# Kernel tuning notes

Hardware: AMD Instinct MI355X
Metric: run time of the kernel (lower is better)

The kernel has to match this reference:

```python
import jax, jax.numpy as jnp
import numpy as np

N_NODES = 50000
NEG_SLOPE = 0.2


def gat_conv(x, src, dst, W, al, ar, b):
    """DGL-style GATConv. x:[N,Fin] W:[Fin,H*D] al,ar:[H,D] b:[H*D] -> [N,H,D]."""
    H, D = al.shape
    feat = (x @ W).reshape(-1, H, D)                      # [N,H,D]
    el = jnp.sum(feat * al, axis=-1)                      # [N,H]
    er = jnp.sum(feat * ar, axis=-1)                      # [N,H]
    e = jax.nn.leaky_relu(el[src] + er[dst], NEG_SLOPE)   # [E,H] per-edge scores
    # segment softmax over incoming edges of each dst node
    m = jax.ops.segment_max(e, dst, num_segments=N_NODES)  # [N,H] (-inf for empty)
    ex = jnp.exp(e - m[dst])                              # [E,H]
    s = jax.ops.segment_sum(ex, dst, num_segments=N_NODES)  # [N,H]
    alpha = ex / s[dst]                                   # [E,H]
    msg = alpha[:, :, None] * feat[src]                   # [E,H,D]
    out = jax.ops.segment_sum(msg, dst, num_segments=N_NODES)  # [N,H,D]
    return out + b.reshape(1, H, D)


def setup_inputs() -> dict:
    key = jax.random.key(0)
    ks = jax.random.split(key, 12)
    E = 800000
    inp = {
        "x": jax.random.normal(ks[0], (N_NODES, 128), jnp.float32),
        "W1": jax.random.normal(ks[1], (2, 128, 128), jnp.float32) * 0.1,
        "al1": jax.random.normal(ks[2], (2, 4, 32), jnp.float32) * 0.1,
        "ar1": jax.random.normal(ks[3], (2, 4, 32), jnp.float32) * 0.1,
        "b1": jnp.zeros((2, 128), jnp.float32),
        "W2": jax.random.normal(ks[4], (2, 128, 64), jnp.float32) * 0.1,
        "al2": jax.random.normal(ks[5], (2, 1, 64), jnp.float32) * 0.1,
        "ar2": jax.random.normal(ks[6], (2, 1, 64), jnp.float32) * 0.1,
        "b2": jnp.zeros((2, 64), jnp.float32),
        "src": jax.random.randint(ks[7], (2, E), 0, N_NODES, jnp.int32),
        "dst": jax.random.randint(ks[8], (2, E), 0, N_NODES, jnp.int32),
    }
    return inp


def reference(x, W1, al1, ar1, b1, W2, al2, ar2, b2, src, dst):
    R = src.shape[0]  # number of meta-path relations
    # layer 1: HeteroGraphConv(sum over relations) -> elu(flatten heads)
    h1 = sum(gat_conv(x, src[r], dst[r], W1[r], al1[r], ar1[r], b1[r])
             for r in range(R))                           # [N,4,32]
    h1 = jax.nn.elu(h1.reshape(N_NODES, -1))              # [N,128]
    # layer 2: single head, mean over head dim
    h2 = sum(gat_conv(h1, src[r], dst[r], W2[r], al2[r], ar2[r], b2[r])
             for r in range(R))                           # [N,1,64]
    return jnp.mean(h2, axis=1)                           # [N,64]
```

## Files before the change

### kernel.cpp

```cpp
#include <hip/hip_runtime.h>
#include <hip/hip_bf16.h>
#include <math.h>

using bf16x8 = __attribute__((ext_vector_type(8))) short;
using f32x4  = __attribute__((ext_vector_type(4))) float;
using v4i    = __attribute__((ext_vector_type(4))) int;

#define NCH 32
#define SCAN_B 1024

__device__ __forceinline__ float b2f(unsigned short u) {
    return __uint_as_float(((unsigned)u) << 16);
}
__device__ __forceinline__ unsigned short f2b(float f) {
    unsigned u = __float_as_uint(f);
    return (unsigned short)((u + 0x7fff + ((u >> 16) & 1)) >> 16);
}

__global__ void k_prep(const float* __restrict__ x, unsigned short* __restrict__ xb, int n8,
                       const float* __restrict__ W1, const float* __restrict__ W2,
                       unsigned short* __restrict__ wt1, unsigned short* __restrict__ wt2,
                       unsigned* __restrict__ cnt, int ncnt, int nbx, int nbw) {
    int bid = blockIdx.x;
    if (bid < nbx) {
        int i = bid * 256 + threadIdx.x;
        if (i >= n8) return;
        float4 a = ((const float4*)x)[i * 2], b = ((const float4*)x)[i * 2 + 1];
        uint4 o;
        o.x = f2b(a.x) | ((unsigned)f2b(a.y) << 16);
        o.y = f2b(a.z) | ((unsigned)f2b(a.w) << 16);
        o.z = f2b(b.x) | ((unsigned)f2b(b.y) << 16);
        o.w = f2b(b.z) | ((unsigned)f2b(b.w) << 16);
        ((uint4*)xb)[i] = o;
    } else if (bid < nbx + nbw) {
        int i = (bid - nbx) * 256 + threadIdx.x;
        if (i < 32768) {
            int r = i >> 14, c = (i >> 7) & 127, k = i & 127;
            wt1[i] = f2b(W1[(r << 14) + (k << 7) + c]);
        } else {
            int j = i - 32768;
            if (j >= 16384) return;
            int r = j >> 13, c = (j >> 7) & 63, k = j & 127;
            wt2[j] = f2b(W2[r * 8192 + k * 64 + c]);
        }
    } else {
        int i = (bid - nbx - nbw) * 256 + threadIdx.x;
        if (i < ncnt) cnt[i] = 0u;
    }
}

__global__ __launch_bounds__(256) void k_histp(const int* __restrict__ dst,
                                               unsigned* __restrict__ cnt, int E, int N) {
    __shared__ unsigned sm[6250];
    const int part = blockIdx.x & 7, chunk = blockIdx.x >> 3;
    const int r = blockIdx.y;
    const int P = N / 8;
    const int lo = part * P;
    for (int i = threadIdx.x; i < P; i += 256) sm[i] = 0u;
    __syncthreads();
    const int per = E / NCH;
    const int e0 = chunk * per, e1 = e0 + per;
    const int* dr = dst + (size_t)r * E;
    for (int e = e0 + (int)threadIdx.x * 4; e < e1; e += 1024) {
        v4i d4 = *(const v4i*)(dr + e);
        int a0 = d4.x - lo, a1 = d4.y - lo, a2 = d4.z - lo, a3 = d4.w - lo;
        if ((unsigned)a0 < (unsigned)P) atomicAdd(&sm[a0], 1u);
        if ((unsigned)a1 < (unsigned)P) atomicAdd(&sm[a1], 1u);
        if ((unsigned)a2 < (unsigned)P) atomicAdd(&sm[a2], 1u);
        if ((unsigned)a3 < (unsigned)P) atomicAdd(&sm[a3], 1u);
    }
    __syncthreads();
    unsigned* cr = cnt + (size_t)r * N + lo;
    for (int i = threadIdx.x; i < P; i += 256) {
        unsigned v = sm[i];
        if (v) atomicAdd(&cr[i], v);
    }
}

__global__ void k_scanA(const unsigned* __restrict__ cnt, unsigned* __restrict__ bsum,
                        int n, int nb) {
    int r = blockIdx.y, b = blockIdx.x;
    int i0 = b * SCAN_B;
    unsigned s = 0;
    for (int t = threadIdx.x; t < SCAN_B; t += 256) {
        int i = i0 + t;
        if (i < n) s += cnt[(size_t)r * n + i];
    }
    __shared__ unsigned red[256];
    red[threadIdx.x] = s; __syncthreads();
    for (int st = 128; st > 0; st >>= 1) {
        if ((int)threadIdx.x < st) red[threadIdx.x] += red[threadIdx.x + st];
        __syncthreads();
    }
    if (threadIdx.x == 0) bsum[r * nb + b] = red[0];
}

__global__ void k_scanC2(unsigned* __restrict__ cnt, const unsigned* __restrict__ bsum,
                         unsigned* __restrict__ off, int n, int nb) {
    int r = blockIdx.y, b = blockIdx.x;
    __shared__ unsigned sbase[65];
    if (threadIdx.x < 64) {
        int l = threadIdx.x;
        unsigned orig = (l < nb) ? bsum[r * nb + l] : 0u;
        unsigned v = orig;
        for (int st = 1; st < 64; st <<= 1) {
            unsigned t = __shfl_up(v, st);
            if (l >= st) v += t;
        }
        sbase[l] = v - orig;
        if (l == 63) sbase[64] = v;
    }
    __syncthreads();
    if (b == 0 && threadIdx.x == 0) off[(size_t)r * (n + 1) + n] = sbase[64];
    const unsigned base = sbase[b];
    int i0 = b * SCAN_B + (int)threadIdx.x * 4;
    unsigned v[4]; unsigned s = 0;
#pragma unroll
    for (int j = 0; j < 4; j++) {
        int i = i0 + j;
        v[j] = (i < n) ? cnt[(size_t)r * n + i] : 0u;
        s += v[j];
    }
    __shared__ unsigned red[256];
    red[threadIdx.x] = s; __syncthreads();
    for (int st = 1; st < 256; st <<= 1) {
        unsigned t = ((int)threadIdx.x >= st) ? red[threadIdx.x - st] : 0u;
        __syncthreads();
        red[threadIdx.x] += t;
        __syncthreads();
    }
    unsigned run = base + red[threadIdx.x] - s;
#pragma unroll
    for (int j = 0; j < 4; j++) {
        int i = i0 + j;
        if (i < n) {
            off[(size_t)r * (n + 1) + i] = run;
            cnt[(size_t)r * n + i] = run;
        }
        run += v[j];
    }
}

__device__ __forceinline__ void scat_body(int bid, const int* __restrict__ src,
                                          const int* __restrict__ dst, unsigned* __restrict__ cur,
                                          unsigned short* __restrict__ csr, int E, int N) {
    const int part = bid & 7;
    const int q = bid >> 3;
    const int r = q & 1, chunk = q >> 1;
    const int lo = part * (N / 8), hi = lo + N / 8;
    const int per = E / NCH;
    const int e0 = chunk * per, e1 = e0 + per;
    const int* dr = dst + (size_t)r * E;
    const int* sr = src + (size_t)r * E;
    unsigned* curr = cur + (size_t)r * N;
    unsigned short* csrr = csr + (size_t)r * E;
    for (int e = e0 + (int)threadIdx.x * 4; e < e1; e += 1024) {
        v4i d4 = *(const v4i*)(dr + e);
        bool m0 = (d4.x >= lo) & (d4.x < hi);
        bool m1 = (d4.y >= lo) & (d4.y < hi);
        bool m2 = (d4.z >= lo) & (d4.z < hi);
        bool m3 = (d4.w >= lo) & (d4.w < hi);
        if (m0 | m1 | m2 | m3) {
            v4i s4 = *(const v4i*)(sr + e);
            if (m0) { unsigned p = atomicAdd(&curr[d4.x], 1u);
                      __builtin_nontemporal_store((unsigned short)s4.x, &csrr[p]); }
            if (m1) { unsigned p = atomicAdd(&curr[d4.y], 1u);
                      __builtin_nontemporal_store((unsigned short)s4.y, &csrr[p]); }
            if (m2) { unsigned p = atomicAdd(&curr[d4.z], 1u);
                      __builtin_nontemporal_store((unsigned short)s4.z, &csrr[p]); }
            if (m3) { unsigned p = atomicAdd(&curr[d4.w], 1u);
                      __builtin_nontemporal_store((unsigned short)s4.w, &csrr[p]); }
        }
    }
}

template <int M, int H>
__device__ __forceinline__ void gemm_body(int xblk, int r,
        const unsigned short* __restrict__ Xb, const unsigned short* __restrict__ Wt0,
        const float* __restrict__ alv, const float* __restrict__ arv,
        unsigned short* __restrict__ feat0, float* __restrict__ el, float* __restrict__ er,
        int N, unsigned short* xs, unsigned short* ws) {
    constexpr int D = M / H;
    const unsigned short* Wt = Wt0 + (size_t)r * M * 128;
    unsigned short* outp = feat0 + (size_t)r * N * M;
    float* elr = el + (size_t)r * N * H;
    float* err = er + (size_t)r * N * H;
    const int tid = threadIdx.x;
    const int row0 = xblk * 64;
    for (int ch = tid; ch < 64 * 16; ch += 256) {
        int rr = ch >> 4, c16 = ch & 15;
        int gr = row0 + rr;
        uint4 v = make_uint4(0, 0, 0, 0);
        if (gr < N) v = ((const uint4*)(Xb + (size_t)gr * 128))[c16];
        int byte = rr * 256 + ((c16 * 16) ^ ((rr & 7) << 4));
        *(uint4*)((char*)xs + byte) = v;
    }
    for (int ch = tid; ch < M * 16; ch += 256) {
        int rr = ch >> 4, c16 = ch & 15;
        uint4 v = ((const uint4*)(Wt + (size_t)rr * 128))[c16];
        int byte = rr * 256 + ((c16 * 16) ^ ((rr & 7) << 4));
        *(uint4*)((char*)ws + byte) = v;
    }
    __syncthreads();
    const int w = tid >> 6, l = tid & 63;
    const int sub = l & 15;
    const int ar_ = w * 16 + sub;
    const int kg = l >> 4;
    bf16x8 a[4];
#pragma unroll
    for (int k4 = 0; k4 < 4; k4++) {
        int byte = ar_ * 256 + (((kg * 16) + k4 * 64) ^ ((ar_ & 7) << 4));
        a[k4] = *(const bf16x8*)((const char*)xs + byte);
    }
    float alr[M / 16], arr[M / 16];
#pragma unroll
    for (int ct = 0; ct < M / 16; ct++) {
        alr[ct] = alv[(size_t)r * M + ct * 16 + sub];
        arr[ct] = arv[(size_t)r * M + ct * 16 + sub];
    }
    float pel[H][4], per[H][4];
#pragma unroll
    for (int h = 0; h < H; h++)
#pragma unroll
        for (int q = 0; q < 4; q++) { pel[h][q] = 0.f; per[h][q] = 0.f; }

#pragma unroll
    for (int ct = 0; ct < M / 16; ct++) {
        f32x4 acc = {0.f, 0.f, 0.f, 0.f};
        const int bc = ct * 16 + sub;
#pragma unroll
        for (int k4 = 0; k4 < 4; k4++) {
            int byte = bc * 256 + (((kg * 16) + k4 * 64) ^ ((bc & 7) << 4));
            bf16x8 bfr = *(const bf16x8*)((const char*)ws + byte);
            acc = __builtin_amdgcn_mfma_f32_16x16x32_bf16(a[k4], bfr, acc, 0, 0, 0);
        }
        const int hct = (ct * 16) / D;
#pragma unroll
        for (int q = 0; q < 4; q++) {
            pel[hct][q] += acc[q] * alr[ct];
            per[hct][q] += acc[q] * arr[ct];
        }
#pragma unroll
        for (int q = 0; q < 4; q++) {
            int gr = row0 + w * 16 + kg * 4 + q;
            if (gr < N) outp[(size_t)gr * M + ct * 16 + sub] = f2b(acc[q]);
        }
    }
#pragma unroll
    for (int h = 0; h < H; h++)
#pragma unroll
        for (int q = 0; q < 4; q++) {
            float v = pel[h][q], u = per[h][q];
#pragma unroll
            for (int o = 8; o > 0; o >>= 1) { v += __shfl_xor(v, o); u += __shfl_xor(u, o); }
            pel[h][q] = v; per[h][q] = u;
        }
#pragma unroll
    for (int h = 0; h < H; h++) {
        if (sub == h) {
#pragma unroll
            for (int q = 0; q < 4; q++) {
                int gr = row0 + w * 16 + kg * 4 + q;
                if (gr < N) { elr[(size_t)gr * H + h] = pel[h][q]; err[(size_t)gr * H + h] = per[h][q]; }
            }
        }
    }
}

__global__ __launch_bounds__(256) void k_scatgemm(
    const int* __restrict__ src, const int* __restrict__ dst,
    unsigned* __restrict__ cur, unsigned short* __restrict__ csr, int E, int N, int scatBlocks,
    const unsigned short* __restrict__ Xb, const unsigned short* __restrict__ Wt0,
    const float* __restrict__ alv, const float* __restrict__ arv,
    unsigned short* __restrict__ feat0, float* __restrict__ el, float* __restrict__ er) {
    __shared__ __align__(16) unsigned short xs[64 * 128];
    __shared__ __align__(16) unsigned short ws[128 * 128];
    int bid = blockIdx.x;
    if (bid < scatBlocks) {
        scat_body(bid, src, dst, cur, csr, E, N);
    } else {
        int g = bid - scatBlocks;
        gemm_body<128, 4>(g >> 1, g & 1, Xb, Wt0, alv, arv, feat0, el, er, N, xs, ws);
    }
}

__global__ __launch_bounds__(256) void k_gemm2(
    const unsigned short* __restrict__ Xb, const unsigned short* __restrict__ Wt0,
    const float* __restrict__ alv, const float* __restrict__ arv,
    unsigned short* __restrict__ feat0, float* __restrict__ el, float* __restrict__ er, int N) {
    __shared__ __align__(16) unsigned short xs[64 * 128];
    __shared__ __align__(16) unsigned short ws[64 * 128];
    gemm_body<64, 1>(blockIdx.x, blockIdx.y, Xb, Wt0, alv, arv, feat0, el, er, N, xs, ws);
}

template <int ELUF>
__global__ __launch_bounds__(256) void k_node_gat1(
    const unsigned* __restrict__ off, const unsigned short* __restrict__ csr_src,
    const float* __restrict__ el, const float* __restrict__ er,
    const unsigned short* __restrict__ feat0, const unsigned short* __restrict__ feat1,
    const float* __restrict__ bias, unsigned* __restrict__ outp, int N, int E) {
    constexpr int H = 4, HD = 128;
    __shared__ float s_w[4][4 * 64];
    __shared__ int s_sid[4][64];
    const int wslot = threadIdx.x >> 6;
    const int lane = threadIdx.x & 63;
    const int n = (blockIdx.x * 256 + threadIdx.x) >> 6;
    if (n >= N) return;
    const int c0 = lane * 2;
    const int h = c0 / 32;
    const unsigned laneoff = (unsigned)lane << 2;

    float res[2] = {0.f, 0.f};

    for (int r = 0; r < 2; r++) {
        const char* __restrict__ featc = (const char*)(r ? feat1 : feat0);
        const float* elr = el + (size_t)r * N * H;
        const float* ernp = er + (size_t)r * N * H + (size_t)n * H;
        float ern[H];
#pragma unroll
        for (int hh = 0; hh < H; hh++) ern[hh] = ernp[hh];
        const unsigned* offr = off + (size_t)r * (N + 1);
        const unsigned short* srcs = csr_src + (size_t)r * E;
        const unsigned o0 = offr[n], o1 = offr[n + 1];

        float den = 0.f;
        float acc[2] = {0.f, 0.f};

        for (unsigned base = o0; base < o1; base += 64) {
            const int cnt = (int)min(64u, o1 - base);
            if (lane < cnt) {
                unsigned sv = srcs[base + lane];
                s_sid[wslot][lane] = (int)sv;
                float4 e4 = *(const float4*)(elr + (size_t)sv * 4);
                float v0 = e4.x + ern[0]; v0 = v0 > 0.f ? v0 : 0.2f * v0;
                float v1 = e4.y + ern[1]; v1 = v1 > 0.f ? v1 : 0.2f * v1;
                float v2 = e4.z + ern[2]; v2 = v2 > 0.f ? v2 : 0.2f * v2;
                float v3 = e4.w + ern[3]; v3 = v3 > 0.f ? v3 : 0.2f * v3;
                float4 wv = make_float4(__expf(v0), __expf(v1), __expf(v2), __expf(v3));
                *(float4*)&s_w[wslot][lane * 4] = wv;
            }
            asm volatile("s_waitcnt lgkmcnt(0)" ::: "memory");
#pragma unroll 8
            for (int j = 0; j < cnt; j++) {
                unsigned sv = (unsigned)s_sid[wslot][j];
                float wv = s_w[wslot][j * 4 + h];
                den += wv;
                unsigned u = *(const unsigned*)(featc + ((sv << 8) + laneoff));
                acc[0] += wv * __uint_as_float(u << 16);
                acc[1] += wv * __uint_as_float(u & 0xffff0000u);
            }
        }
        if (den > 0.f) {
            float inv = 1.f / den;
            res[0] += acc[0] * inv;
            res[1] += acc[1] * inv;
        }
    }
    float v0 = res[0] + bias[c0] + bias[HD + c0];
    float v1 = res[1] + bias[c0 + 1] + bias[HD + c0 + 1];
    if (ELUF) { v0 = v0 > 0.f ? v0 : expm1f(v0); v1 = v1 > 0.f ? v1 : expm1f(v1); }
    outp[((size_t)n * HD + c0) / 2] = f2b(v0) | ((unsigned)f2b(v1) << 16);
}

__global__ __launch_bounds__(256) void k_node_gat2(
    const unsigned* __restrict__ off, const unsigned short* __restrict__ csr_src,
    const float* __restrict__ el, const float* __restrict__ er,
    const unsigned short* __restrict__ feat0, const unsigned short* __restrict__ feat1,
    const float* __restrict__ bias, float* __restrict__ outp, int N, int E) {
    __shared__ uint2 s_ws[4][64];
    const int wslot = threadIdx.x >> 6;
    const int lane = threadIdx.x & 63;
    const int n = (blockIdx.x * 256 + threadIdx.x) >> 6;
    if (n >= N) return;
    const int sub = lane & 31, half = lane >> 5;
    const unsigned laneoff = (unsigned)sub << 2;

    float res[2] = {0.f, 0.f};

    for (int r = 0; r < 2; r++) {
        const char* __restrict__ featc = (const char*)(r ? feat1 : feat0);
        const float* elr = el + (size_t)r * N;
        const float ern = er[(size_t)r * N + n];
        const unsigned* offr = off + (size_t)r * (N + 1);
        const unsigned short* srcs = csr_src + (size_t)r * E;
        const unsigned o0 = offr[n], o1 = offr[n + 1];

        float den = 0.f;
        float acc[2] = {0.f, 0.f};

        for (unsigned base = o0; base < o1; base += 64) {
            const int cnt = (int)min(64u, o1 - base);
            if (lane < cnt) {
                unsigned sv = srcs[base + lane];
                float v = elr[sv] + ern; v = v > 0.f ? v : 0.2f * v;
                s_ws[wslot][lane] = make_uint2(sv, __float_as_uint(__expf(v)));
            }
            asm volatile("s_waitcnt lgkmcnt(0)" ::: "memory");
#pragma unroll 4
            for (int j2 = 0; j2 < cnt; j2 += 2) {
                int jj = j2 + half;
                int jjc = jj < cnt ? jj : 0;
                uint2 sw = s_ws[wslot][jjc];
                float wv = (jj < cnt) ? __uint_as_float(sw.y) : 0.f;
                den += wv;
                unsigned u = *(const unsigned*)(featc + (((size_t)sw.x << 7) + laneoff));
                acc[0] += wv * __uint_as_float(u << 16);
                acc[1] += wv * __uint_as_float(u & 0xffff0000u);
            }
        }
        acc[0] += __shfl_xor(acc[0], 32);
        acc[1] += __shfl_xor(acc[1], 32);
        den += __shfl_xor(den, 32);
        if (den > 0.f) {
            float inv = 1.f / den;
            res[0] += acc[0] * inv;
            res[1] += acc[1] * inv;
        }
    }
    if (half == 0) {
        int c = sub * 2;
        float v0 = res[0] + bias[c] + bias[64 + c];
        float v1 = res[1] + bias[c + 1] + bias[64 + c + 1];
        *(float2*)(outp + (size_t)n * 64 + c) = make_float2(v0, v1);
    }
}

extern "C" void kernel_launch(void* const* d_in, const int* in_sizes, int n_in,
                              void* d_out, int out_size, void* d_ws, size_t ws_size,
                              hipStream_t stream) {
    const float* x   = (const float*)d_in[0];
    const float* W1  = (const float*)d_in[1];
    const float* al1 = (const float*)d_in[2];
    const float* ar1 = (const float*)d_in[3];
    const float* b1  = (const float*)d_in[4];
    const float* W2  = (const float*)d_in[5];
    const float* al2 = (const float*)d_in[6];
    const float* ar2 = (const float*)d_in[7];
    const float* b2  = (const float*)d_in[8];
    const int* src   = (const int*)d_in[9];
    const int* dst   = (const int*)d_in[10];

    const int N = in_sizes[0] / 128;
    const int E = in_sizes[9] / 2;
    float* out = (float*)d_out;

    char* w = (char*)d_ws;
    unsigned short* xb   = (unsigned short*)w; w += (size_t)N * 128 * 2;
    unsigned short* feat = (unsigned short*)w; w += (size_t)2 * N * 128 * 2;
    unsigned short* h1b  = (unsigned short*)w; w += (size_t)N * 128 * 2;
    unsigned short* wt1  = (unsigned short*)w; w += (size_t)2 * 128 * 128 * 2;
    unsigned short* wt2  = (unsigned short*)w; w += (size_t)2 * 64 * 128 * 2;
    float* el      = (float*)w; w += (size_t)2 * N * 4 * 4;
    float* er      = (float*)w; w += (size_t)2 * N * 4 * 4;
    unsigned* cnt  = (unsigned*)w; w += (size_t)2 * N * 4;
    unsigned* off  = (unsigned*)w; w += (size_t)2 * (N + 1) * 4;
    unsigned* bsum = (unsigned*)w; w += 2 * 64 * 4;
    unsigned short* csr_src = (unsigned short*)w; w += (size_t)2 * E * 2;

    auto cdiv = [](long long a, long long b) { return (int)((a + b - 1) / b); };
    const int NB = cdiv(N, SCAN_B);

    const int nbx = cdiv((long long)N * 16, 256);
    const int nbw = cdiv(49152, 256);
    const int nbz = cdiv(2LL * N, 256);
    k_prep<<<nbx + nbw + nbz, 256, 0, stream>>>(x, xb, N * 16, W1, W2, wt1, wt2, cnt, 2 * N, nbx, nbw);

    { dim3 g(NCH * 8, 2); k_histp<<<g, 256, 0, stream>>>(dst, cnt, E, N); }
    { dim3 g(NB, 2); k_scanA<<<g, 256, 0, stream>>>(cnt, bsum, N, NB); }
    { dim3 g(NB, 2); k_scanC2<<<g, 256, 0, stream>>>(cnt, bsum, off, N, NB); }

    const int scatBlocks = NCH * 8 * 2;
    const int gemmBlocks = cdiv(N, 64) * 2;
    k_scatgemm<<<scatBlocks + gemmBlocks, 256, 0, stream>>>(
        src, dst, cnt, csr_src, E, N, scatBlocks, xb, wt1, al1, ar1, feat, el, er);

    k_node_gat1<1><<<cdiv(N, 4), 256, 0, stream>>>(off, csr_src, el, er,
        feat, feat + (size_t)N * 128, b1, (unsigned*)h1b, N, E);

    { dim3 g(cdiv(N, 64), 2);
      k_gemm2<<<g, 256, 0, stream>>>(h1b, wt2, al2, ar2, feat, el, er, N); }
    k_node_gat2<<<cdiv(N, 4), 256, 0, stream>>>(off, csr_src, el, er,
        feat, feat + (size_t)N * 64, b2, out, N, E);
}
```

Measured before the change: 244.7 us.

## Process four edges per wave in layer-2 aggregation and raise scatter chunk count

The layer-2 node aggregation kernel now splits each 64-lane wave into four 16-lane groups. Each lane loads 8 bytes (four bf16 features) per edge, so four edges are handled per iteration instead of two. The partial sums are then reduced with two cross-lane shuffles and written back as float4. Separately, NCH is doubled to 64, which changes the scatter/GEMM block count and chunking in the hidden kernel, while the histogram kernel is pinned to the old 32 chunks. This raises the number of edge loads in flight per wave but adds a shuffle step and may change scatter behaviour.

After: 255.6 us. 1.04x slower.

```diff
diff --git a/kernel.cpp b/kernel.cpp
--- a/kernel.cpp
+++ b/kernel.cpp
@@ -6,7 +6,7 @@
 using f32x4  = __attribute__((ext_vector_type(4))) float;
 using v4i    = __attribute__((ext_vector_type(4))) int;
 
-#define NCH 32
+#define NCH 64
 #define SCAN_B 1024
 
 __device__ __forceinline__ float b2f(unsigned short u) {
@@ -58,7 +58,7 @@
     const int lo = part * P;
     for (int i = threadIdx.x; i < P; i += 256) sm[i] = 0u;
     __syncthreads();
-    const int per = E / NCH;
+    const int per = E / 32;
     const int e0 = chunk * per, e1 = e0 + per;
     const int* dr = dst + (size_t)r * E;
     for (int e = e0 + (int)threadIdx.x * 4; e < e1; e += 1024) {
@@ -372,10 +372,10 @@
     const int lane = threadIdx.x & 63;
     const int n = (blockIdx.x * 256 + threadIdx.x) >> 6;
     if (n >= N) return;
-    const int sub = lane & 31, half = lane >> 5;
-    const unsigned laneoff = (unsigned)sub << 2;
-
-    float res[2] = {0.f, 0.f};
+    const int sub = lane & 15, quarter = lane >> 4;
+    const unsigned laneoff = (unsigned)sub << 3;
+
+    float res[4] = {0.f, 0.f, 0.f, 0.f};
 
     for (int r = 0; r < 2; r++) {
         const char* __restrict__ featc = (const char*)(r ? feat1 : feat0);
@@ -386,7 +386,7 @@
         const unsigned o0 = offr[n], o1 = offr[n + 1];
 
         float den = 0.f;
-        float acc[2] = {0.f, 0.f};
+        float acc[4] = {0.f, 0.f, 0.f, 0.f};
 
         for (unsigned base = o0; base < o1; base += 64) {
             const int cnt = (int)min(64u, o1 - base);
@@ -397,31 +397,40 @@
             }
             asm volatile("s_waitcnt lgkmcnt(0)" ::: "memory");
 #pragma unroll 4
-            for (int j2 = 0; j2 < cnt; j2 += 2) {
-                int jj = j2 + half;
+            for (int j4 = 0; j4 < cnt; j4 += 4) {
+                int jj = j4 + quarter;
                 int jjc = jj < cnt ? jj : 0;
                 uint2 sw = s_ws[wslot][jjc];
                 float wv = (jj < cnt) ? __uint_as_float(sw.y) : 0.f;
                 den += wv;
-                unsigned u = *(const unsigned*)(featc + (((size_t)sw.x << 7) + laneoff));
-                acc[0] += wv * __uint_as_float(u << 16);
-                acc[1] += wv * __uint_as_float(u & 0xffff0000u);
+                uint2 u = *(const uint2*)(featc + (((size_t)sw.x << 7) + laneoff));
+                acc[0] += wv * __uint_as_float(u.x << 16);
+                acc[1] += wv * __uint_as_float(u.x & 0xffff0000u);
+                acc[2] += wv * __uint_as_float(u.y << 16);
+                acc[3] += wv * __uint_as_float(u.y & 0xffff0000u);
             }
         }
-        acc[0] += __shfl_xor(acc[0], 32);
-        acc[1] += __shfl_xor(acc[1], 32);
+#pragma unroll
+        for (int f = 0; f < 4; f++) {
+            acc[f] += __shfl_xor(acc[f], 16);
+            acc[f] += __shfl_xor(acc[f], 32);
+        }
+        den += __shfl_xor(den, 16);
         den += __shfl_xor(den, 32);
         if (den > 0.f) {
             float inv = 1.f / den;
-            res[0] += acc[0] * inv;
-            res[1] += acc[1] * inv;
-        }
-    }
-    if (half == 0) {
-        int c = sub * 2;
-        float v0 = res[0] + bias[c] + bias[64 + c];
-        float v1 = res[1] + bias[c + 1] + bias[64 + c + 1];
-        *(float2*)(outp + (size_t)n * 64 + c) = make_float2(v0, v1);
+#pragma unroll
+            for (int f = 0; f < 4; f++) res[f] += acc[f] * inv;
+        }
+    }
+    if (quarter == 0) {
+        int c = sub * 4;
+        float4 o;
+        o.x = res[0] + bias[c] + bias[64 + c];
+        o.y = res[1] + bias[c + 1] + bias[64 + c + 1];
+        o.z = res[2] + bias[c + 2] + bias[64 + c + 2];
+        o.w = res[3] + bias[c + 3] + bias[64 + c + 3];
+        *(float4*)(outp + (size_t)n * 64 + c) = o;
     }
 }
 
@@ -465,7 +474,7 @@
     const int nbz = cdiv(2LL * N, 256);
     k_prep<<<nbx + nbw + nbz, 256, 0, stream>>>(x, xb, N * 16, W1, W2, wt1, wt2, cnt, 2 * N, nbx, nbw);
 
-    { dim3 g(NCH * 8, 2); k_histp<<<g, 256, 0, stream>>>(dst, cnt, E, N); }
+    { dim3 g(32 * 8, 2); k_histp<<<g, 256, 0, stream>>>(dst, cnt, E, N); }
     { dim3 g(NB, 2); k_scanA<<<g, 256, 0, stream>>>(cnt, bsum, N, NB); }
     { dim3 g(NB, 2); k_scanC2<<<g, 256, 0, stream>>>(cnt, bsum, off, N, NB); }
 
```
